# Kernel tuning notes

Measured on AMD Instinct MI355X. Metric: run time of the kernel, lower is better.

Reference implementation:

```python
import jax, jax.numpy as jnp
import numpy as np

BETA = 0.25
EPS = 1e-12  # matches torch F.normalize eps


def _normalize(x):
    # L2-normalize along last dim, matching F.normalize(x, dim=1)
    n = jnp.linalg.norm(x, axis=-1, keepdims=True)
    return x / jnp.maximum(n, EPS)


def setup_inputs() -> dict:
    key = jax.random.key(0)
    k1, k2 = jax.random.split(key)
    B, C, H, W = 32, 256, 32, 32
    num_embed = 8192
    z = jax.random.normal(k1, (B, C, H, W), dtype=jnp.float32)
    # codebook initialized uniform(-1/K, 1/K) as in the module
    embed_weight = jax.random.uniform(
        k2, (num_embed, C), minval=-1.0 / num_embed, maxval=1.0 / num_embed,
        dtype=jnp.float32)
    return {"z": z, "embed_weight": embed_weight}


def reference(z, embed_weight):
    B, C, H, W = z.shape
    sg = jax.lax.stop_gradient
    zt = jnp.transpose(z, (0, 2, 3, 1))           # [B, H, W, C]
    zf = zt.reshape(-1, C)                         # [N, C]
    # cosine distance (dot of normalized vectors); z side is detached
    zn = sg(_normalize(zf))                        # [N, C]
    cn = _normalize(embed_weight)                  # [K, C]
    dist = jnp.einsum('nd,kd->nk', zn, cn)         # [N, K]
    encoding_indices = jnp.argmax(dist, axis=1)    # [N]
    z_q = embed_weight[encoding_indices].reshape(zt.shape)  # [B, H, W, C]
    loss = (BETA * jnp.mean((sg(z_q) - zt) ** 2)
            + jnp.mean((z_q - sg(zt)) ** 2))
    z_q_st = zt + sg(z_q - zt)                     # straight-through
    out = jnp.transpose(z_q_st, (0, 3, 1, 2))      # [B, C, H, W]
    return out, loss, encoding_indices
```

## Files before the change

### kernel.cpp

```cpp
#include <hip/hip_runtime.h>
#include <hip/hip_bf16.h>

#define NROWS 32768
#define CDIM  256
#define KCODES 8192
#define HWPB  1024
#define OUT_ELEMS 8388608
#define KSPLIT 4

__global__ __launch_bounds__(256) void vq_invnorm_kernel(
    const float* __restrict__ e, float* __restrict__ invn) {
  const int row  = blockIdx.x * 4 + (threadIdx.x >> 6);
  const int lane = threadIdx.x & 63;
  const float4 v = *reinterpret_cast<const float4*>(e + (size_t)row * CDIM + lane * 4);
  float s = v.x * v.x + v.y * v.y + v.z * v.z + v.w * v.w;
  #pragma unroll
  for (int o = 32; o > 0; o >>= 1) s += __shfl_down(s, o);
  if (lane == 0) invn[row] = 1.0f / fmaxf(sqrtf(s), 1e-12f);
}

#define BM 128
#define BN 128
#define KC 16

__global__ __launch_bounds__(256) void vq_dist_argmax_kernel(
    const float* __restrict__ z, const float* __restrict__ e,
    const float* __restrict__ invn,
    float* __restrict__ bestval, int* __restrict__ bestidx) {
  __shared__ float as[KC][BM];
  __shared__ float bs[KC][BN + 4];

  const int t  = threadIdx.x;
  const int tx = t & 15;
  const int ty = t >> 4;
  const int n0 = blockIdx.x * BM;
  const int b   = n0 >> 10;
  const int hw0 = n0 & 1023;
  const float* zbase = z + (size_t)b * (CDIM * HWPB) + hw0;
  const int kbeg = blockIdx.y * (KCODES / KSPLIT);

  float bv[8]; int bi[8];
  #pragma unroll
  for (int i = 0; i < 8; ++i) { bv[i] = -3.4e38f; bi[i] = 0; }

  const int a_lm4 = (t & 31) * 4;
  const int a_cc  = t >> 5;
  const int b_kk  = t >> 2;
  const int b_q4  = (t & 3) * 4;

  for (int kt = 0; kt < (KCODES / KSPLIT) / BN; ++kt) {
    const int k0 = kbeg + kt * BN;
    float acc[8][8];
    #pragma unroll
    for (int i = 0; i < 8; ++i)
      #pragma unroll
      for (int j = 0; j < 8; ++j) acc[i][j] = 0.f;

    for (int c0 = 0; c0 < CDIM; c0 += KC) {
      #pragma unroll
      for (int p = 0; p < 2; ++p) {
        const int cc = a_cc + 8 * p;
        const float4 v = *reinterpret_cast<const float4*>(
            zbase + (size_t)(c0 + cc) * HWPB + a_lm4);
        *reinterpret_cast<float4*>(&as[cc][a_lm4]) = v;
      }
      #pragma unroll
      for (int p = 0; p < 2; ++p) {
        const int kk = b_kk + 64 * p;
        const float4 v = *reinterpret_cast<const float4*>(
            e + (size_t)(k0 + kk) * CDIM + c0 + b_q4);
        bs[b_q4 + 0][kk] = v.x;
        bs[b_q4 + 1][kk] = v.y;
        bs[b_q4 + 2][kk] = v.z;
        bs[b_q4 + 3][kk] = v.w;
      }
      __syncthreads();
      #pragma unroll
      for (int cc = 0; cc < KC; ++cc) {
        const float4 a0 = *reinterpret_cast<const float4*>(&as[cc][ty * 8]);
        const float4 a1 = *reinterpret_cast<const float4*>(&as[cc][ty * 8 + 4]);
        const float4 b0 = *reinterpret_cast<const float4*>(&bs[cc][tx * 4]);
        const float4 b1 = *reinterpret_cast<const float4*>(&bs[cc][64 + tx * 4]);
        const float a[8]  = {a0.x, a0.y, a0.z, a0.w, a1.x, a1.y, a1.z, a1.w};
        const float bb[8] = {b0.x, b0.y, b0.z, b0.w, b1.x, b1.y, b1.z, b1.w};
        #pragma unroll
        for (int i = 0; i < 8; ++i)
          #pragma unroll
          for (int j = 0; j < 8; ++j)
            acc[i][j] = fmaf(a[i], bb[j], acc[i][j]);
      }
      __syncthreads();
    }

    #pragma unroll
    for (int j = 0; j < 8; ++j) {
      const int k = k0 + ((j < 4) ? (tx * 4 + j) : (64 + tx * 4 + (j - 4)));
      const float inv = invn[k];
      #pragma unroll
      for (int i = 0; i < 8; ++i) {
        const float v = acc[i][j] * inv;
        if (v > bv[i]) { bv[i] = v; bi[i] = k; }
      }
    }
  }

  #pragma unroll
  for (int m = 1; m < 16; m <<= 1) {
    #pragma unroll
    for (int i = 0; i < 8; ++i) {
      const float vo = __shfl_xor(bv[i], m);
      const int   io = __shfl_xor(bi[i], m);
      if (vo > bv[i] || (vo == bv[i] && io < bi[i])) { bv[i] = vo; bi[i] = io; }
    }
  }
  if (tx == 0) {
    #pragma unroll
    for (int i = 0; i < 8; ++i) {
      bestval[blockIdx.y * NROWS + n0 + ty * 8 + i] = bv[i];
      bestidx[blockIdx.y * NROWS + n0 + ty * 8 + i] = bi[i];
    }
  }
}

__global__ __launch_bounds__(256) void vq_gather_loss_kernel(
    const float* __restrict__ z, const float* __restrict__ e,
    const float* __restrict__ bestval, const int* __restrict__ bestidx,
    float* __restrict__ out, float* __restrict__ lossacc) {
  __shared__ int sidx[64];
  const int t  = threadIdx.x;
  const int n0 = blockIdx.x * 64;
  if (t < 64) {
    const int n = n0 + t;
    float best = bestval[n];
    int   bid  = bestidx[n];
    #pragma unroll
    for (int p = 1; p < KSPLIT; ++p) {
      const float v = bestval[p * NROWS + n];
      const int  id = bestidx[p * NROWS + n];
      if (v > best) { best = v; bid = id; }
    }
    sidx[t] = bid;
    out[OUT_ELEMS + 1 + n] = (float)bid;
  }
  __syncthreads();
  const int b    = n0 >> 10;
  const int hw0  = n0 & 1023;
  const int nsub = t & 63;
  const int cg   = t >> 6;
  const float* erow = e + (size_t)sidx[nsub] * CDIM;
  float lsum = 0.f;
  for (int c = cg; c < CDIM; c += 4) {
    const float  v   = erow[c];
    const size_t off = (size_t)b * (CDIM * HWPB) + (size_t)c * HWPB + hw0 + nsub;
    const float  d   = v - z[off];
    lsum += d * d;
    out[off] = v;
  }
  #pragma unroll
  for (int o = 32; o > 0; o >>= 1) lsum += __shfl_down(lsum, o);
  __shared__ float wsum[4];
  if ((t & 63) == 0) wsum[t >> 6] = lsum;
  __syncthreads();
  if (t == 0) atomicAdd(lossacc, wsum[0] + wsum[1] + wsum[2] + wsum[3]);
}

__global__ void vq_finalize_kernel(const float* __restrict__ lossacc,
                                   float* __restrict__ out) {
  out[OUT_ELEMS] = 1.25f * lossacc[0] / (float)OUT_ELEMS;
}

extern "C" void kernel_launch(void* const* d_in, const int* in_sizes, int n_in,
                              void* d_out, int out_size, void* d_ws, size_t ws_size,
                              hipStream_t stream) {
  const float* z = (const float*)d_in[0];
  const float* e = (const float*)d_in[1];
  float* out = (float*)d_out;

  float* invn    = (float*)d_ws;
  float* bestval = invn + KCODES;
  int*   bestidx = (int*)(bestval + KSPLIT * NROWS);
  float* lossacc = (float*)(bestidx + KSPLIT * NROWS);

  hipMemsetAsync(lossacc, 0, sizeof(float), stream);

  vq_invnorm_kernel<<<KCODES / 4, 256, 0, stream>>>(e, invn);

  dim3 grid(NROWS / BM, KSPLIT);
  vq_dist_argmax_kernel<<<grid, 256, 0, stream>>>(z, e, invn, bestval, bestidx);

  vq_gather_loss_kernel<<<NROWS / 64, 256, 0, stream>>>(z, e, bestval, bestidx,
                                                        out, lossacc);
  vq_finalize_kernel<<<1, 1, 0, stream>>>(lossacc, out);
}
```

Before: 1.681 ms.

## Use split-bf16 MFMA GEMM with top-2 margin rescoring for VQ argmax

Replaces the fp32 SIMT distance GEMM with a bf16 MFMA kernel. It splits z and the codebook into hi/lo bf16 pairs (hi*hi + hi*lo + lo*hi across 12 K-chunks) and loads tiles into LDS directly from global memory with XOR swizzling. The kernel tracks the top-2 scores per row. Rows whose margin is below a threshold are flagged and re-scored in exact fp32 against the full codebook. Inputs are pre-transposed and converted by separate prep kernels. The old path is kept as a fallback when the workspace is too small. This risks wrong indices if the approximation error exceeds the threshold, and the extra prep and rescore kernels add cost.

After: 2.029 ms. +20.7%, slower.

```diff
diff --git a/kernel.cpp b/kernel.cpp
--- a/kernel.cpp
+++ b/kernel.cpp
@@ -1,12 +1,27 @@
 #include <hip/hip_runtime.h>
-#include <hip/hip_bf16.h>
 
 #define NROWS 32768
 #define CDIM  256
 #define KCODES 8192
 #define HWPB  1024
 #define OUT_ELEMS 8388608
-#define KSPLIT 4
+
+typedef unsigned short ushort_t;
+typedef unsigned int uint_t;
+typedef __attribute__((ext_vector_type(8))) __bf16 bf16x8;
+typedef __attribute__((ext_vector_type(4))) float f32x4;
+typedef __attribute__((ext_vector_type(8))) ushort_t us8;
+typedef __attribute__((ext_vector_type(4))) ushort_t us4;
+
+#define RESCORE_THRESH 1.0e-3f
+
+__device__ __forceinline__ ushort_t f2bf(float f) {
+  uint_t u = __float_as_uint(f);
+  return (ushort_t)((u + 0x7fffu + ((u >> 16) & 1u)) >> 16);
+}
+__device__ __forceinline__ float bf2f(ushort_t s) {
+  return __uint_as_float(((uint_t)s) << 16);
+}
 
 __global__ __launch_bounds__(256) void vq_invnorm_kernel(
     const float* __restrict__ e, float* __restrict__ invn) {
@@ -19,128 +34,297 @@
   if (lane == 0) invn[row] = 1.0f / fmaxf(sqrtf(s), 1e-12f);
 }
 
-#define BM 128
-#define BN 128
-#define KC 16
-
-__global__ __launch_bounds__(256) void vq_dist_argmax_kernel(
+__global__ __launch_bounds__(256) void vq_prep_b_kernel(
+    const float* __restrict__ e, ushort_t* __restrict__ B2) {
+  const int k  = blockIdx.x * 4 + (threadIdx.x >> 6);
+  const int ln = threadIdx.x & 63;
+  const float4 v = reinterpret_cast<const float4*>(e + (size_t)k * CDIM)[ln];
+  us4 hi, lo;
+  const float vv[4] = {v.x, v.y, v.z, v.w};
+  #pragma unroll
+  for (int i = 0; i < 4; ++i) {
+    ushort_t h = f2bf(vv[i]);
+    hi[i] = h;
+    lo[i] = f2bf(vv[i] - bf2f(h));
+  }
+  *reinterpret_cast<us4*>(B2 + (size_t)k * 512 + ln * 4)       = hi;
+  *reinterpret_cast<us4*>(B2 + (size_t)k * 512 + 256 + ln * 4) = lo;
+}
+
+__global__ __launch_bounds__(256) void vq_prep_a_kernel(
+    const float* __restrict__ z, ushort_t* __restrict__ A2) {
+  __shared__ float zt[64][65];
+  const int t    = threadIdx.x;
+  const int bidx = blockIdx.x;
+  const int b    = bidx >> 6;
+  const int cblk = (bidx & 63) >> 4;
+  const int hwb  = bidx & 15;
+  const int c0   = cblk * 64;
+  const int hw0  = hwb * 64;
+  #pragma unroll
+  for (int rep = 0; rep < 16; ++rep) {
+    const int idx = rep * 256 + t;
+    const int cc = idx >> 6, hh = idx & 63;
+    zt[cc][hh] = z[(size_t)(b * 256 + c0 + cc) * 1024 + hw0 + hh];
+  }
+  __syncthreads();
+  const int r = t >> 2, q = t & 3;
+  const int n = b * 1024 + hw0 + r;
+  us8 hi0, hi1, lo0, lo1;
+  #pragma unroll
+  for (int m2 = 0; m2 < 16; ++m2) {
+    const float v = zt[q * 16 + m2][r];
+    const ushort_t h = f2bf(v);
+    const ushort_t l = f2bf(v - bf2f(h));
+    if (m2 < 8) { hi0[m2] = h; lo0[m2] = l; } else { hi1[m2 - 8] = h; lo1[m2 - 8] = l; }
+  }
+  ushort_t* hrow = A2 + (size_t)n * 512 + c0 + q * 16;
+  ushort_t* lrow = A2 + (size_t)n * 512 + 256 + c0 + q * 16;
+  *reinterpret_cast<us8*>(hrow)     = hi0;
+  *reinterpret_cast<us8*>(hrow + 8) = hi1;
+  *reinterpret_cast<us8*>(lrow)     = lo0;
+  *reinterpret_cast<us8*>(lrow + 8) = lo1;
+}
+
+__global__ __launch_bounds__(256) void vq_mfma_kernel(
+    const ushort_t* __restrict__ A2, const ushort_t* __restrict__ B2,
+    const float* __restrict__ invn,
+    float* __restrict__ partV1, int* __restrict__ partI1,
+    float* __restrict__ partV2) {
+  __shared__ __align__(16) char As[16384];
+  __shared__ __align__(16) char Bs[16384];
+
+  const int t = threadIdx.x;
+  const int w = t >> 6, l = t & 63;
+  const int wr = w >> 1, wc = w & 1;
+  const int lane15 = l & 15, kg = l >> 4;
+  const int m0 = blockIdx.x * 128;
+  const int cg = blockIdx.y;
+
+  const int lr = l >> 3;
+  const int lc = (l & 7) ^ lr;
+
+  float bv[16], b2v[16]; int bi[16];
+  #pragma unroll
+  for (int iq = 0; iq < 16; ++iq) { bv[iq] = -3.4e38f; b2v[iq] = -3.4e38f; bi[iq] = 0; }
+
+  for (int nt = 0; nt < 8; ++nt) {
+    const int nbase = cg * 1024 + nt * 128;
+    f32x4 acc[4][4];
+    #pragma unroll
+    for (int i = 0; i < 4; ++i)
+      #pragma unroll
+      for (int j = 0; j < 4; ++j) acc[i][j] = (f32x4){0.f, 0.f, 0.f, 0.f};
+
+    for (int kc = 0; kc < 12; ++kc) {
+      const int seg = kc >> 2, rem = (kc & 3) * 64;
+      const int aoff = (seg == 1 ? 256 : 0) + rem;
+      const int boff = (seg == 2 ? 256 : 0) + rem;
+      #pragma unroll
+      for (int p = 0; p < 4; ++p) {
+        const int r = p * 32 + w * 8 + lr;
+        __builtin_amdgcn_global_load_lds(
+            (const __attribute__((address_space(1))) void*)(A2 + (size_t)(m0 + r) * 512 + aoff + lc * 8),
+            (__attribute__((address_space(3))) void*)(As + (p * 32 + w * 8) * 128), 16, 0, 0);
+        __builtin_amdgcn_global_load_lds(
+            (const __attribute__((address_space(1))) void*)(B2 + (size_t)(nbase + r) * 512 + boff + lc * 8),
+            (__attribute__((address_space(3))) void*)(Bs + (p * 32 + w * 8) * 128), 16, 0, 0);
+      }
+      __syncthreads();
+      #pragma unroll
+      for (int kk = 0; kk < 2; ++kk) {
+        bf16x8 af[4], bfr[4];
+        const int sw = kk * 64 + kg * 16;
+        const int sx = (lane15 & 7) << 4;
+        #pragma unroll
+        for (int i = 0; i < 4; ++i) {
+          const int row = wr * 64 + i * 16 + lane15;
+          af[i] = *reinterpret_cast<const bf16x8*>(As + row * 128 + (sw ^ sx));
+        }
+        #pragma unroll
+        for (int j = 0; j < 4; ++j) {
+          const int row = wc * 64 + j * 16 + lane15;
+          bfr[j] = *reinterpret_cast<const bf16x8*>(Bs + row * 128 + (sw ^ sx));
+        }
+        #pragma unroll
+        for (int i = 0; i < 4; ++i)
+          #pragma unroll
+          for (int j = 0; j < 4; ++j)
+            acc[i][j] = __builtin_amdgcn_mfma_f32_16x16x32_bf16(af[i], bfr[j], acc[i][j], 0, 0, 0);
+      }
+      __syncthreads();
+    }
+
+    float inv4[4];
+    #pragma unroll
+    for (int j = 0; j < 4; ++j) inv4[j] = invn[nbase + wc * 64 + j * 16 + lane15];
+    #pragma unroll
+    for (int i = 0; i < 4; ++i)
+      #pragma unroll
+      for (int q = 0; q < 4; ++q) {
+        const int iq = i * 4 + q;
+        #pragma unroll
+        for (int j = 0; j < 4; ++j) {
+          const float v = acc[i][j][q] * inv4[j];
+          const int k = nbase + wc * 64 + j * 16 + lane15;
+          if (v > bv[iq]) { b2v[iq] = bv[iq]; bv[iq] = v; bi[iq] = k; }
+          else if (v > b2v[iq]) b2v[iq] = v;
+        }
+      }
+  }
+
+  #pragma unroll
+  for (int m = 1; m < 16; m <<= 1) {
+    #pragma unroll
+    for (int iq = 0; iq < 16; ++iq) {
+      const float ov = __shfl_xor(bv[iq], m);
+      const int   oi = __shfl_xor(bi[iq], m);
+      const float o2 = __shfl_xor(b2v[iq], m);
+      const float n2 = fmaxf(fmaxf(b2v[iq], o2), fminf(bv[iq], ov));
+      if (ov > bv[iq] || (ov == bv[iq] && oi < bi[iq])) { bv[iq] = ov; bi[iq] = oi; }
+      b2v[iq] = n2;
+    }
+  }
+
+  float* lv1 = reinterpret_cast<float*>(As);
+  float* lv2 = lv1 + 128;
+  int*   li1 = reinterpret_cast<int*>(lv2 + 128);
+  if (wc == 1 && lane15 == 0) {
+    #pragma unroll
+    for (int i = 0; i < 4; ++i)
+      #pragma unroll
+      for (int q = 0; q < 4; ++q) {
+        const int rl = wr * 64 + i * 16 + kg * 4 + q;
+        lv1[rl] = bv[i * 4 + q]; lv2[rl] = b2v[i * 4 + q]; li1[rl] = bi[i * 4 + q];
+      }
+  }
+  __syncthreads();
+  if (wc == 0 && lane15 == 0) {
+    #pragma unroll
+    for (int i = 0; i < 4; ++i)
+      #pragma unroll
+      for (int q = 0; q < 4; ++q) {
+        const int iq = i * 4 + q;
+        const int rl = wr * 64 + i * 16 + kg * 4 + q;
+        const float ov = lv1[rl]; const float o2 = lv2[rl]; const int oi = li1[rl];
+        const float n2 = fmaxf(fmaxf(b2v[iq], o2), fminf(bv[iq], ov));
+        float v1 = bv[iq]; int i1 = bi[iq];
+        if (ov > v1 || (ov == v1 && oi < i1)) { v1 = ov; i1 = oi; }
+        const size_t g = (size_t)cg * NROWS + m0 + rl;
+        partV1[g] = v1; partI1[g] = i1; partV2[g] = n2;
+      }
+  }
+}
+
+__global__ __launch_bounds__(256) void vq_merge_flag_kernel(
+    const float* __restrict__ partV1, const int* __restrict__ partI1,
+    const float* __restrict__ partV2,
+    int* __restrict__ final_idx, int* __restrict__ flag, int* __restrict__ cnt) {
+  const int n = blockIdx.x * 256 + threadIdx.x;
+  float v1 = partV1[n]; int i1 = partI1[n]; float v2 = partV2[n];
+  #pragma unroll
+  for (int cg = 1; cg < 8; ++cg) {
+    const float pv1 = partV1[(size_t)cg * NROWS + n];
+    const int   pi1 = partI1[(size_t)cg * NROWS + n];
+    const float pv2 = partV2[(size_t)cg * NROWS + n];
+    const float n2 = fmaxf(fmaxf(v2, pv2), fminf(v1, pv1));
+    if (pv1 > v1) { v1 = pv1; i1 = pi1; }
+    v2 = n2;
+  }
+  final_idx[n] = i1;
+  if (v1 - v2 < RESCORE_THRESH) {
+    const int p = atomicAdd(cnt, 1);
+    flag[p] = n;
+  }
+}
+
+__global__ __launch_bounds__(256) void vq_rescore_kernel(
     const float* __restrict__ z, const float* __restrict__ e,
-    const float* __restrict__ invn,
-    float* __restrict__ bestval, int* __restrict__ bestidx) {
-  __shared__ float as[KC][BM];
-  __shared__ float bs[KC][BN + 4];
-
-  const int t  = threadIdx.x;
-  const int tx = t & 15;
-  const int ty = t >> 4;
-  const int n0 = blockIdx.x * BM;
-  const int b   = n0 >> 10;
-  const int hw0 = n0 & 1023;
-  const float* zbase = z + (size_t)b * (CDIM * HWPB) + hw0;
-  const int kbeg = blockIdx.y * (KCODES / KSPLIT);
-
-  float bv[8]; int bi[8];
-  #pragma unroll
-  for (int i = 0; i < 8; ++i) { bv[i] = -3.4e38f; bi[i] = 0; }
-
-  const int a_lm4 = (t & 31) * 4;
-  const int a_cc  = t >> 5;
-  const int b_kk  = t >> 2;
-  const int b_q4  = (t & 3) * 4;
-
-  for (int kt = 0; kt < (KCODES / KSPLIT) / BN; ++kt) {
-    const int k0 = kbeg + kt * BN;
-    float acc[8][8];
-    #pragma unroll
-    for (int i = 0; i < 8; ++i)
-      #pragma unroll
-      for (int j = 0; j < 8; ++j) acc[i][j] = 0.f;
-
-    for (int c0 = 0; c0 < CDIM; c0 += KC) {
-      #pragma unroll
-      for (int p = 0; p < 2; ++p) {
-        const int cc = a_cc + 8 * p;
-        const float4 v = *reinterpret_cast<const float4*>(
-            zbase + (size_t)(c0 + cc) * HWPB + a_lm4);
-        *reinterpret_cast<float4*>(&as[cc][a_lm4]) = v;
-      }
-      #pragma unroll
-      for (int p = 0; p < 2; ++p) {
-        const int kk = b_kk + 64 * p;
-        const float4 v = *reinterpret_cast<const float4*>(
-            e + (size_t)(k0 + kk) * CDIM + c0 + b_q4);
-        bs[b_q4 + 0][kk] = v.x;
-        bs[b_q4 + 1][kk] = v.y;
-        bs[b_q4 + 2][kk] = v.z;
-        bs[b_q4 + 3][kk] = v.w;
-      }
-      __syncthreads();
-      #pragma unroll
-      for (int cc = 0; cc < KC; ++cc) {
-        const float4 a0 = *reinterpret_cast<const float4*>(&as[cc][ty * 8]);
-        const float4 a1 = *reinterpret_cast<const float4*>(&as[cc][ty * 8 + 4]);
-        const float4 b0 = *reinterpret_cast<const float4*>(&bs[cc][tx * 4]);
-        const float4 b1 = *reinterpret_cast<const float4*>(&bs[cc][64 + tx * 4]);
-        const float a[8]  = {a0.x, a0.y, a0.z, a0.w, a1.x, a1.y, a1.z, a1.w};
-        const float bb[8] = {b0.x, b0.y, b0.z, b0.w, b1.x, b1.y, b1.z, b1.w};
+    const float* __restrict__ invn, const int* __restrict__ cnt,
+    const int* __restrict__ flag, int* __restrict__ final_idx) {
+  __shared__ float zr[8][256];
+  __shared__ int rows[8];
+  __shared__ float redv[8][4];
+  __shared__ int   redi[8][4];
+  const int t = threadIdx.x;
+  const int total = *cnt;
+  for (int base = blockIdx.x * 8; base < total; base += gridDim.x * 8) {
+    const int nr = min(8, total - base);
+    __syncthreads();
+    if (t < 8) rows[t] = (base + t < total) ? flag[base + t] : flag[base];
+    __syncthreads();
+    for (int rr = 0; rr < 8; ++rr) {
+      if (rr < nr) {
+        const int n = rows[rr];
+        const int b = n >> 10, hw = n & 1023;
+        zr[rr][t] = z[(size_t)b * 262144 + (size_t)t * 1024 + hw];
+      } else {
+        zr[rr][t] = 0.f;
+      }
+    }
+    __syncthreads();
+    float bvv[8]; int bii[8];
+    #pragma unroll
+    for (int rr = 0; rr < 8; ++rr) { bvv[rr] = -3.4e38f; bii[rr] = 0; }
+    for (int jj = 0; jj < 32; ++jj) {
+      const int k = t * 32 + jj;
+      const float4* er = reinterpret_cast<const float4*>(e + (size_t)k * CDIM);
+      float d[8];
+      #pragma unroll
+      for (int rr = 0; rr < 8; ++rr) d[rr] = 0.f;
+      for (int c4 = 0; c4 < 64; ++c4) {
+        const float4 ev = er[c4];
         #pragma unroll
-        for (int i = 0; i < 8; ++i)
-          #pragma unroll
-          for (int j = 0; j < 8; ++j)
-            acc[i][j] = fmaf(a[i], bb[j], acc[i][j]);
-      }
-      __syncthreads();
-    }
-
-    #pragma unroll
-    for (int j = 0; j < 8; ++j) {
-      const int k = k0 + ((j < 4) ? (tx * 4 + j) : (64 + tx * 4 + (j - 4)));
+        for (int rr = 0; rr < 8; ++rr) {
+          d[rr] = fmaf(ev.x, zr[rr][c4 * 4 + 0], d[rr]);
+          d[rr] = fmaf(ev.y, zr[rr][c4 * 4 + 1], d[rr]);
+          d[rr] = fmaf(ev.z, zr[rr][c4 * 4 + 2], d[rr]);
+          d[rr] = fmaf(ev.w, zr[rr][c4 * 4 + 3], d[rr]);
+        }
+      }
       const float inv = invn[k];
       #pragma unroll
-      for (int i = 0; i < 8; ++i) {
-        const float v = acc[i][j] * inv;
-        if (v > bv[i]) { bv[i] = v; bi[i] = k; }
-      }
-    }
-  }
-
-  #pragma unroll
-  for (int m = 1; m < 16; m <<= 1) {
-    #pragma unroll
-    for (int i = 0; i < 8; ++i) {
-      const float vo = __shfl_xor(bv[i], m);
-      const int   io = __shfl_xor(bi[i], m);
-      if (vo > bv[i] || (vo == bv[i] && io < bi[i])) { bv[i] = vo; bi[i] = io; }
-    }
-  }
-  if (tx == 0) {
-    #pragma unroll
-    for (int i = 0; i < 8; ++i) {
-      bestval[blockIdx.y * NROWS + n0 + ty * 8 + i] = bv[i];
-      bestidx[blockIdx.y * NROWS + n0 + ty * 8 + i] = bi[i];
-    }
-  }
-}
-
-__global__ __launch_bounds__(256) void vq_gather_loss_kernel(
+      for (int rr = 0; rr < 8; ++rr) {
+        const float v = d[rr] * inv;
+        if (v > bvv[rr]) { bvv[rr] = v; bii[rr] = k; }
+      }
+    }
+    #pragma unroll
+    for (int m = 1; m < 64; m <<= 1) {
+      #pragma unroll
+      for (int rr = 0; rr < 8; ++rr) {
+        const float ov = __shfl_xor(bvv[rr], m);
+        const int   oi = __shfl_xor(bii[rr], m);
+        if (ov > bvv[rr] || (ov == bvv[rr] && oi < bii[rr])) { bvv[rr] = ov; bii[rr] = oi; }
+      }
+    }
+    if ((t & 63) == 0) {
+      #pragma unroll
+      for (int rr = 0; rr < 8; ++rr) { redv[rr][t >> 6] = bvv[rr]; redi[rr][t >> 6] = bii[rr]; }
+    }
+    __syncthreads();
+    if (t < nr) {
+      float v = redv[t][0]; int i = redi[t][0];
+      #pragma unroll
+      for (int ww = 1; ww < 4; ++ww) {
+        if (redv[t][ww] > v || (redv[t][ww] == v && redi[t][ww] < i)) { v = redv[t][ww]; i = redi[t][ww]; }
+      }
+      final_idx[rows[t]] = i;
+    }
+  }
+}
+
+__global__ __launch_bounds__(256) void vq_gather_loss2_kernel(
     const float* __restrict__ z, const float* __restrict__ e,
-    const float* __restrict__ bestval, const int* __restrict__ bestidx,
+    const int* __restrict__ final_idx,
     float* __restrict__ out, float* __restrict__ lossacc) {
   __shared__ int sidx[64];
   const int t  = threadIdx.x;
   const int n0 = blockIdx.x * 64;
   if (t < 64) {
-    const int n = n0 + t;
-    float best = bestval[n];
-    int   bid  = bestidx[n];
-    #pragma unroll
-    for (int p = 1; p < KSPLIT; ++p) {
-      const float v = bestval[p * NROWS + n];
-      const int  id = bestidx[p * NROWS + n];
-      if (v > best) { best = v; bid = id; }
-    }
-    sidx[t] = bid;
-    out[OUT_ELEMS + 1 + n] = (float)bid;
+    const int id = final_idx[n0 + t];
+    sidx[t] = id;
+    out[OUT_ELEMS + 1 + n0 + t] = (float)id;
   }
   __syncthreads();
   const int b    = n0 >> 10;
@@ -169,6 +353,145 @@
   out[OUT_ELEMS] = 1.25f * lossacc[0] / (float)OUT_ELEMS;
 }
 
+#define BM 128
+#define BN 128
+#define KC 16
+#define KSPLIT 4
+
+__global__ __launch_bounds__(256) void vq_dist_argmax_kernel(
+    const float* __restrict__ z, const float* __restrict__ e,
+    const float* __restrict__ invn,
+    float* __restrict__ bestval, int* __restrict__ bestidx) {
+  __shared__ float as[KC][BM];
+  __shared__ float bs[KC][BN + 4];
+  const int t  = threadIdx.x;
+  const int tx = t & 15;
+  const int ty = t >> 4;
+  const int n0 = blockIdx.x * BM;
+  const int b   = n0 >> 10;
+  const int hw0 = n0 & 1023;
+  const float* zbase = z + (size_t)b * (CDIM * HWPB) + hw0;
+  const int kbeg = blockIdx.y * (KCODES / KSPLIT);
+  float bv[8]; int bi[8];
+  #pragma unroll
+  for (int i = 0; i < 8; ++i) { bv[i] = -3.4e38f; bi[i] = 0; }
+  const int a_lm4 = (t & 31) * 4;
+  const int a_cc  = t >> 5;
+  const int b_kk  = t >> 2;
+  const int b_q4  = (t & 3) * 4;
+  for (int kt = 0; kt < (KCODES / KSPLIT) / BN; ++kt) {
+    const int k0 = kbeg + kt * BN;
+    float acc[8][8];
+    #pragma unroll
+    for (int i = 0; i < 8; ++i)
+      #pragma unroll
+      for (int j = 0; j < 8; ++j) acc[i][j] = 0.f;
+    for (int c0 = 0; c0 < CDIM; c0 += KC) {
+      #pragma unroll
+      for (int p = 0; p < 2; ++p) {
+        const int cc = a_cc + 8 * p;
+        const float4 v = *reinterpret_cast<const float4*>(
+            zbase + (size_t)(c0 + cc) * HWPB + a_lm4);
+        *reinterpret_cast<float4*>(&as[cc][a_lm4]) = v;
+      }
+      #pragma unroll
+      for (int p = 0; p < 2; ++p) {
+        const int kk = b_kk + 64 * p;
+        const float4 v = *reinterpret_cast<const float4*>(
+            e + (size_t)(k0 + kk) * CDIM + c0 + b_q4);
+        bs[b_q4 + 0][kk] = v.x;
+        bs[b_q4 + 1][kk] = v.y;
+        bs[b_q4 + 2][kk] = v.z;
+        bs[b_q4 + 3][kk] = v.w;
+      }
+      __syncthreads();
+      #pragma unroll
+      for (int cc = 0; cc < KC; ++cc) {
+        const float4 a0 = *reinterpret_cast<const float4*>(&as[cc][ty * 8]);
+        const float4 a1 = *reinterpret_cast<const float4*>(&as[cc][ty * 8 + 4]);
+        const float4 b0 = *reinterpret_cast<const float4*>(&bs[cc][tx * 4]);
+        const float4 b1 = *reinterpret_cast<const float4*>(&bs[cc][64 + tx * 4]);
+        const float a[8]  = {a0.x, a0.y, a0.z, a0.w, a1.x, a1.y, a1.z, a1.w};
+        const float bb[8] = {b0.x, b0.y, b0.z, b0.w, b1.x, b1.y, b1.z, b1.w};
+        #pragma unroll
+        for (int i = 0; i < 8; ++i)
+          #pragma unroll
+          for (int j = 0; j < 8; ++j)
+            acc[i][j] = fmaf(a[i], bb[j], acc[i][j]);
+      }
+      __syncthreads();
+    }
+    #pragma unroll
+    for (int j = 0; j < 8; ++j) {
+      const int k = k0 + ((j < 4) ? (tx * 4 + j) : (64 + tx * 4 + (j - 4)));
+      const float inv = invn[k];
+      #pragma unroll
+      for (int i = 0; i < 8; ++i) {
+        const float v = acc[i][j] * inv;
+        if (v > bv[i]) { bv[i] = v; bi[i] = k; }
+      }
+    }
+  }
+  #pragma unroll
+  for (int m = 1; m < 16; m <<= 1) {
+    #pragma unroll
+    for (int i = 0; i < 8; ++i) {
+      const float vo = __shfl_xor(bv[i], m);
+      const int   io = __shfl_xor(bi[i], m);
+      if (vo > bv[i] || (vo == bv[i] && io < bi[i])) { bv[i] = vo; bi[i] = io; }
+    }
+  }
+  if (tx == 0) {
+    #pragma unroll
+    for (int i = 0; i < 8; ++i) {
+      bestval[blockIdx.y * NROWS + n0 + ty * 8 + i] = bv[i];
+      bestidx[blockIdx.y * NROWS + n0 + ty * 8 + i] = bi[i];
+    }
+  }
+}
+
+__global__ __launch_bounds__(256) void vq_gather_loss_kernel(
+    const float* __restrict__ z, const float* __restrict__ e,
+    const float* __restrict__ bestval, const int* __restrict__ bestidx,
+    float* __restrict__ out, float* __restrict__ lossacc) {
+  __shared__ int sidx[64];
+  const int t  = threadIdx.x;
+  const int n0 = blockIdx.x * 64;
+  if (t < 64) {
+    const int n = n0 + t;
+    float best = bestval[n];
+    int   bid  = bestidx[n];
+    #pragma unroll
+    for (int p = 1; p < KSPLIT; ++p) {
+      const float v = bestval[p * NROWS + n];
+      const int  id = bestidx[p * NROWS + n];
+      if (v > best) { best = v; bid = id; }
+    }
+    sidx[t] = bid;
+    out[OUT_ELEMS + 1 + n] = (float)bid;
+  }
+  __syncthreads();
+  const int b    = n0 >> 10;
+  const int hw0  = n0 & 1023;
+  const int nsub = t & 63;
+  const int cg   = t >> 6;
+  const float* erow = e + (size_t)sidx[nsub] * CDIM;
+  float lsum = 0.f;
+  for (int c = cg; c < CDIM; c += 4) {
+    const float  v   = erow[c];
+    const size_t off = (size_t)b * (CDIM * HWPB) + (size_t)c * HWPB + hw0 + nsub;
+    const float  d   = v - z[off];
+    lsum += d * d;
+    out[off] = v;
+  }
+  #pragma unroll
+  for (int o = 32; o > 0; o >>= 1) lsum += __shfl_down(lsum, o);
+  __shared__ float wsum[4];
+  if ((t & 63) == 0) wsum[t >> 6] = lsum;
+  __syncthreads();
+  if (t == 0) atomicAdd(lossacc, wsum[0] + wsum[1] + wsum[2] + wsum[3]);
+}
+
 extern "C" void kernel_launch(void* const* d_in, const int* in_sizes, int n_in,
                               void* d_out, int out_size, void* d_ws, size_t ws_size,
                               hipStream_t stream) {
@@ -176,19 +499,47 @@
   const float* e = (const float*)d_in[1];
   float* out = (float*)d_out;
 
-  float* invn    = (float*)d_ws;
-  float* bestval = invn + KCODES;
-  int*   bestidx = (int*)(bestval + KSPLIT * NROWS);
-  float* lossacc = (float*)(bestidx + KSPLIT * NROWS);
-
-  hipMemsetAsync(lossacc, 0, sizeof(float), stream);
-
-  vq_invnorm_kernel<<<KCODES / 4, 256, 0, stream>>>(e, invn);
-
-  dim3 grid(NROWS / BM, KSPLIT);
-  vq_dist_argmax_kernel<<<grid, 256, 0, stream>>>(z, e, invn, bestval, bestidx);
-
-  vq_gather_loss_kernel<<<NROWS / 64, 256, 0, stream>>>(z, e, bestval, bestidx,
-                                                        out, lossacc);
-  vq_finalize_kernel<<<1, 1, 0, stream>>>(lossacc, out);
-}
+  const size_t szA2 = (size_t)NROWS * 512 * 2;
+  const size_t szB2 = (size_t)KCODES * 512 * 2;
+  const size_t szInv = KCODES * 4;
+  const size_t szPart = (size_t)8 * NROWS * 4;
+  const size_t need = szA2 + szB2 + szInv + 3 * szPart + 2 * (size_t)NROWS * 4 + 256;
+
+  if (ws_size >= need) {
+    char* p = (char*)d_ws;
+    ushort_t* A2 = (ushort_t*)p;       p += szA2;
+    ushort_t* B2 = (ushort_t*)p;       p += szB2;
+    float* invn  = (float*)p;          p += szInv;
+    float* partV1 = (float*)p;         p += szPart;
+    float* partV2 = (float*)p;         p += szPart;
+    int*   partI1 = (int*)p;           p += szPart;
+    int*   final_idx = (int*)p;        p += (size_t)NROWS * 4;
+    int*   flag = (int*)p;             p += (size_t)NROWS * 4;
+    int*   cnt = (int*)p;
+    float* lossacc = (float*)(cnt + 1);
+
+    hipMemsetAsync(cnt, 0, 8, stream);
+    vq_invnorm_kernel<<<KCODES / 4, 256, 0, stream>>>(e, invn);
+    vq_prep_b_kernel<<<KCODES / 4, 256, 0, stream>>>(e, B2);
+    vq_prep_a_kernel<<<2048, 256, 0, stream>>>(z, A2);
+    dim3 grid(NROWS / 128, 8);
+    vq_mfma_kernel<<<grid, 256, 0, stream>>>(A2, B2, invn, partV1, partI1, partV2);
+    vq_merge_flag_kernel<<<NROWS / 256, 256, 0, stream>>>(partV1, partI1, partV2,
+                                                          final_idx, flag, cnt);
+    vq_rescore_kernel<<<256, 256, 0, stream>>>(z, e, invn, cnt, flag, final_idx);
+    vq_gather_loss2_kernel<<<NROWS / 64, 256, 0, stream>>>(z, e, final_idx, out, lossacc);
+    vq_finalize_kernel<<<1, 1, 0, stream>>>(lossacc, out);
+  } else {
+    float* invn    = (float*)d_ws;
+    float* bestval = invn + KCODES;
+    int*   bestidx = (int*)(bestval + KSPLIT * NROWS);
+    float* lossacc = (float*)(bestidx + KSPLIT * NROWS);
+    hipMemsetAsync(lossacc, 0, sizeof(float), stream);
+    vq_invnorm_kernel<<<KCODES / 4, 256, 0, stream>>>(e, invn);
+    dim3 grid(NROWS / BM, KSPLIT);
+    vq_dist_argmax_kernel<<<grid, 256, 0, stream>>>(z, e, invn, bestval, bestidx);
+    vq_gather_loss_kernel<<<NROWS / 64, 256, 0, stream>>>(z, e, bestval, bestidx,
+                                                          out, lossacc);
+    vq_finalize_kernel<<<1, 1, 0, stream>>>(lossacc, out);
+  }
+}
```
